# Optimization experiments

Hardware: AMD Instinct MI355X
Metric: run time of the kernel (lower is better)

## Reference

```python
import jax, jax.numpy as jnp
import numpy as np

D_MODEL = 1024
N_HEADS = 16
HEAD_DIM = D_MODEL // N_HEADS
ROPE_BASE = 10000.0


def setup_inputs() -> dict:
    key = jax.random.key(0)
    ks = jax.random.split(key, 9)
    s = 0.02
    inp = {
        "x": jax.random.normal(ks[0], (2, 2048, D_MODEL), dtype=jnp.float32),
        "Wq": jax.random.normal(ks[1], (D_MODEL, D_MODEL), dtype=jnp.float32) * s,
        "bq": jnp.zeros((D_MODEL,), dtype=jnp.float32),
        "Wk": jax.random.normal(ks[2], (D_MODEL, D_MODEL), dtype=jnp.float32) * s,
        "bk": jnp.zeros((D_MODEL,), dtype=jnp.float32),
        "Wv": jax.random.normal(ks[3], (D_MODEL, D_MODEL), dtype=jnp.float32) * s,
        "bv": jnp.zeros((D_MODEL,), dtype=jnp.float32),
        "Wo": jax.random.normal(ks[4], (D_MODEL, D_MODEL), dtype=jnp.float32) * s,
        "bo": jnp.zeros((D_MODEL,), dtype=jnp.float32),
    }
    return inp


def _rope_cos_sin(T, head_dim, dtype):
    inv_freq = 1.0 / (ROPE_BASE ** (jnp.arange(0, head_dim, 2, dtype=jnp.float32) / head_dim))
    pos = jnp.arange(T, dtype=jnp.float32)
    freqs = jnp.outer(pos, inv_freq)              # [T, head_dim/2]
    emb = jnp.concatenate([freqs, freqs], axis=-1)  # [T, head_dim]
    return jnp.cos(emb).astype(dtype), jnp.sin(emb).astype(dtype)


def _rotate_half(x):
    x1, x2 = jnp.split(x, 2, axis=-1)
    return jnp.concatenate([-x2, x1], axis=-1)


def reference(x, Wq, bq, Wk, bk, Wv, bv, Wo, bo):
    B, T, _ = x.shape
    H, Dh = N_HEADS, HEAD_DIM
    # projections (torch Linear: x @ W.T + b)
    q = (x @ Wq.T + bq).reshape(B, T, H, Dh).transpose(0, 2, 1, 3)  # [B,H,T,Dh]
    k = (x @ Wk.T + bk).reshape(B, T, H, Dh).transpose(0, 2, 1, 3)
    v = (x @ Wv.T + bv).reshape(B, T, H, Dh).transpose(0, 2, 1, 3)
    cos, sin = _rope_cos_sin(T, Dh, x.dtype)  # [T, Dh]
    cos = cos[None, None]
    sin = sin[None, None]
    q = q * cos + _rotate_half(q) * sin
    k = k * cos + _rotate_half(k) * sin
    scale = 1.0 / jnp.sqrt(jnp.asarray(Dh, dtype=x.dtype))
    attn = jnp.einsum("bhqd,bhkd->bhqk", q, k) * scale
    attn = jax.nn.softmax(attn, axis=-1)
    out = jnp.einsum("bhqk,bhkd->bhqd", attn, v)  # [B,H,T,Dh]
    out = out.transpose(0, 2, 1, 3).reshape(B, T, H * Dh)
    return out @ Wo.T + bo
```

## Files before the change

kernel.cpp:

```cpp
#include <hip/hip_runtime.h>
#include <hip/hip_bf16.h>
#include <cstdint>

#define D_MODEL 1024
#define NHEADS 16
#define HDIM 64
#define SEQ 2048
#define NBATCH 2
#define BT (NBATCH * SEQ)

typedef short bf16x8 __attribute__((ext_vector_type(8)));
typedef float f32x4 __attribute__((ext_vector_type(4)));
typedef unsigned short u16;
typedef unsigned int u32;

__device__ inline u16 f2bf(float f) {
    union { float f; u32 u; } x;
    x.f = f;
    u32 r = (x.u + 0x7fffu + ((x.u >> 16) & 1u)) >> 16;
    return (u16)r;
}

__device__ inline u32 pack2bf(float a, float b) {
    union { __hip_bfloat162 h; u32 u; } c;
    c.h = __float22bfloat162_rn(float2{a, b});
    return c.u;
}

__device__ inline float bf2f(u16 v) {
    union { u32 u; float f; } x;
    x.u = ((u32)v) << 16;
    return x.f;
}

__device__ inline void async_copy16(const u16* g, u16* l) {
    __builtin_amdgcn_global_load_lds((const __attribute__((address_space(1))) void*)g,
                                     (__attribute__((address_space(3))) void*)l, 16, 0, 0);
}

#define X4 (BT * D_MODEL / 4)
#define W4 (D_MODEL * D_MODEL / 4)
#define ROPE_N (SEQ * 32)

__global__ void prep_kernel(const float* __restrict__ x,
                            const float* __restrict__ wq, const float* __restrict__ wk,
                            const float* __restrict__ wv, const float* __restrict__ wo,
                            u16* __restrict__ xb,
                            u16* __restrict__ dq, u16* __restrict__ dk,
                            u16* __restrict__ dv, u16* __restrict__ dow,
                            float* __restrict__ cosT, float* __restrict__ sinT) {
    int idx = blockIdx.x * blockDim.x + threadIdx.x;
    if (idx < X4) {
        float4 v = ((const float4*)x)[idx];
        ushort4 o;
        o.x = f2bf(v.x); o.y = f2bf(v.y); o.z = f2bf(v.z); o.w = f2bf(v.w);
        ((ushort4*)xb)[idx] = o;
    } else if (idx < X4 + 4 * W4) {
        int j = idx - X4;
        int w = j >> 18, i = j & (W4 - 1);
        const float* s = (w == 0) ? wq : (w == 1) ? wk : (w == 2) ? wv : wo;
        u16* d = (w == 0) ? dq : (w == 1) ? dk : (w == 2) ? dv : dow;
        float4 v = ((const float4*)s)[i];
        ushort4 o;
        o.x = f2bf(v.x); o.y = f2bf(v.y); o.z = f2bf(v.z); o.w = f2bf(v.w);
        ((ushort4*)d)[i] = o;
    } else {
        int j = idx - (X4 + 4 * W4);
        if (j < ROPE_N) {
            int t = j >> 5, dd = j & 31;
            float invf = exp2f(-(float)dd * (13.287712379549449f / 32.0f));
            float ang = (float)t * invf;
            float s, c;
            sincosf(ang, &s, &c);
            cosT[t * HDIM + dd] = c;      cosT[t * HDIM + dd + 32] = c;
            sinT[t * HDIM + dd] = s;      sinT[t * HDIM + dd + 32] = s;
        }
    }
}

__device__ inline void gemm_tile_core(const u16* __restrict__ A, const u16* __restrict__ Bw,
                                      int blkM, int blkN,
                                      u16* Asmem, u16* Bsmem, f32x4 acc[4][4]) {
    const int tid = threadIdx.x;
    const int lane = tid & 63;
    const int wave = tid >> 6;
    const int waveM = wave >> 1, waveN = wave & 1;
    const int quad = lane >> 4, l16 = lane & 15;

    const int srow = tid >> 2;
    const int scol = (tid & 3) << 3;
    const u16* Ag0 = A + (size_t)(blkM * 128 + srow) * D_MODEL + scol;
    const u16* Ag1 = Ag0 + (size_t)64 * D_MODEL;
    const u16* Bg0 = Bw + (size_t)(blkN * 128 + srow) * D_MODEL + scol;
    const u16* Bg1 = Bg0 + (size_t)64 * D_MODEL;
    u16* Al0 = Asmem + srow * 32 + scol;
    u16* Al1 = Al0 + 64 * 32;
    u16* Bl0 = Bsmem + srow * 32 + scol;
    u16* Bl1 = Bl0 + 64 * 32;

    for (int k0 = 0; k0 < D_MODEL; k0 += 32) {
        __syncthreads();
        async_copy16(Ag0 + k0, Al0);
        async_copy16(Ag1 + k0, Al1);
        async_copy16(Bg0 + k0, Bl0);
        async_copy16(Bg1 + k0, Bl1);
        __syncthreads();
        bf16x8 af[4], bfr[4];
#pragma unroll
        for (int mt = 0; mt < 4; ++mt)
            af[mt] = *(const bf16x8*)&Asmem[(waveM * 64 + mt * 16 + l16) * 32 + quad * 8];
#pragma unroll
        for (int nt = 0; nt < 4; ++nt)
            bfr[nt] = *(const bf16x8*)&Bsmem[(waveN * 64 + nt * 16 + l16) * 32 + quad * 8];
#pragma unroll
        for (int mt = 0; mt < 4; ++mt)
#pragma unroll
            for (int nt = 0; nt < 4; ++nt)
                acc[mt][nt] = __builtin_amdgcn_mfma_f32_16x16x32_bf16(af[mt], bfr[nt], acc[mt][nt], 0, 0, 0);
    }
}

#define QSCALE 0.1803368801111204f
#define VPAD 132

__global__ __launch_bounds__(256) void gemm_qkv_kernel(
    const u16* __restrict__ xb,
    const u16* __restrict__ wqb, const u16* __restrict__ wkb, const u16* __restrict__ wvb,
    const float* __restrict__ bq, const float* __restrict__ bk, const float* __restrict__ bv,
    const float* __restrict__ cosT, const float* __restrict__ sinT,
    u16* __restrict__ Qb, u16* __restrict__ Kb, u16* __restrict__ VTb) {
    __shared__ __align__(16) u16 smem[128 * VPAD];
    u16* Asmem = smem;
    u16* Bsmem = smem + 128 * 32;

    const int z = blockIdx.z;
    const u16* Bw = (z == 0) ? wqb : (z == 1) ? wkb : wvb;
    const float* bias = (z == 0) ? bq : (z == 1) ? bk : bv;

    f32x4 acc[4][4];
#pragma unroll
    for (int mt = 0; mt < 4; ++mt)
#pragma unroll
        for (int nt = 0; nt < 4; ++nt)
            acc[mt][nt] = (f32x4){0.f, 0.f, 0.f, 0.f};

    gemm_tile_core(xb, Bw, blockIdx.x, blockIdx.y, Asmem, Bsmem, acc);

    const int tid = threadIdx.x;
    const int lane = tid & 63, wave = tid >> 6;
    const int waveM = wave >> 1, waveN = wave & 1;
    const int quad = lane >> 4, l16 = lane & 15;
    const int gm0 = blockIdx.x * 128 + waveM * 64 + quad * 4;
    const int gn0 = blockIdx.y * 128 + waveN * 64 + l16;

    float bvv[4];
#pragma unroll
    for (int nt = 0; nt < 4; ++nt) bvv[nt] = bias[gn0 + nt * 16];
#pragma unroll
    for (int mt = 0; mt < 4; ++mt)
#pragma unroll
        for (int nt = 0; nt < 4; ++nt)
#pragma unroll
            for (int r = 0; r < 4; ++r) acc[mt][nt][r] += bvv[nt];

    if (z < 2) {
        u16* dst = (z == 0) ? Qb : Kb;
        const float post = (z == 0) ? QSCALE : 1.0f;
#pragma unroll
        for (int mt = 0; mt < 4; ++mt) {
#pragma unroll
            for (int nt = 0; nt < 4; ++nt) {
                int n = gn0 + nt * 16;
                int d = n & 63, h = n >> 6;
#pragma unroll
                for (int r = 0; r < 4; ++r) {
                    int gm = gm0 + mt * 16 + r;
                    int t = gm & (SEQ - 1), b = gm >> 11;
                    float c = cosT[t * HDIM + d], s = sinT[t * HDIM + d];
                    float part = acc[mt][nt ^ 2][r];
                    float rot = (d < 32) ? -part : part;
                    float val = (acc[mt][nt][r] * c + rot * s) * post;
                    dst[((b * NHEADS + h) * SEQ + t) * HDIM + d] = f2bf(val);
                }
            }
        }
    } else {
        __syncthreads();
#pragma unroll
        for (int mt = 0; mt < 4; ++mt) {
            int t_local = waveM * 64 + mt * 16 + quad * 4;
#pragma unroll
            for (int nt = 0; nt < 4; ++nt) {
                int n_local = waveN * 64 + nt * 16 + l16;
                uint2 w;
                w.x = pack2bf(acc[mt][nt][0], acc[mt][nt][1]);
                w.y = pack2bf(acc[mt][nt][2], acc[mt][nt][3]);
                *(uint2*)&smem[n_local * VPAD + t_local] = w;
            }
        }
        __syncthreads();
        const int row = tid >> 1;
        const int hc = (tid & 1) * 64;
        const int n_g = blockIdx.y * 128 + row;
        const int h = n_g >> 6, d = n_g & 63;
        const int b = (blockIdx.x * 128) >> 11;
        const int t0 = ((blockIdx.x * 128) & (SEQ - 1)) + hc;
        u16* dst = &VTb[((size_t)(b * NHEADS + h) * HDIM + d) * SEQ + t0];
        const u16* src = &smem[row * VPAD + hc];
#pragma unroll
        for (int j = 0; j < 8; ++j)
            *(int4*)&dst[j * 8] = *(const int4*)&src[j * 8];
    }
}

#define LPAD 72

__global__ __launch_bounds__(256, 1) void flash_kernel(
    const u16* __restrict__ Qb, const u16* __restrict__ Kb, const u16* __restrict__ VTb,
    u16* __restrict__ Po0, u16* __restrict__ Po1, float* __restrict__ Ls) {
    __shared__ __align__(16) u16 Ks[64 * LPAD];
    __shared__ __align__(16) u16 VTs[64 * LPAD];
    __shared__ __align__(16) u16 Ps[4][64 * LPAD];

    const int tid = threadIdx.x;
    const int wave = tid >> 6, lane = tid & 63;
    const int quad = lane >> 4, l16 = lane & 15;
    const int bh = blockIdx.y;
    const int hf = blockIdx.z;
    const u16* Qh = Qb + (size_t)bh * SEQ * HDIM;
    const u16* Kh = Kb + (size_t)bh * SEQ * HDIM;
    const u16* Vh = VTb + (size_t)bh * HDIM * SEQ;
    const int qblk = blockIdx.x * 256 + wave * 64;
    u16* Pw = (u16*)Ps[wave];

    bf16x8 aq[4][2];
#pragma unroll
    for (int nt2 = 0; nt2 < 4; ++nt2)
#pragma unroll
        for (int ks = 0; ks < 2; ++ks)
            aq[nt2][ks] = *(const bf16x8*)&Qh[(qblk + nt2 * 16 + l16) * HDIM + ks * 32 + quad * 8];

    f32x4 o[4][4];
    float lsum[4] = {0.f, 0.f, 0.f, 0.f};
#pragma unroll
    for (int mt2 = 0; mt2 < 4; ++mt2)
#pragma unroll
        for (int nt = 0; nt < 4; ++nt) o[mt2][nt] = (f32x4){0.f, 0.f, 0.f, 0.f};

    const int lr = tid >> 2;
    const int lc = (tid & 3) * 16;

    const int ktEnd = (hf + 1) * (SEQ / 128);
    for (int kt = hf * (SEQ / 128); kt < ktEnd; ++kt) {
        __syncthreads();
        *(int4*)&Ks[lr * LPAD + lc] = *(const int4*)&Kh[(kt * 64 + lr) * HDIM + lc];
        *(int4*)&Ks[lr * LPAD + lc + 8] = *(const int4*)&Kh[(kt * 64 + lr) * HDIM + lc + 8];
        *(int4*)&VTs[lr * LPAD + lc] = *(const int4*)&Vh[lr * SEQ + kt * 64 + lc];
        *(int4*)&VTs[lr * LPAD + lc + 8] = *(const int4*)&Vh[lr * SEQ + kt * 64 + lc + 8];
        __syncthreads();

        f32x4 sacc[4][4];
#pragma unroll
        for (int mt = 0; mt < 4; ++mt)
#pragma unroll
            for (int nt2 = 0; nt2 < 4; ++nt2) sacc[mt][nt2] = (f32x4){0.f, 0.f, 0.f, 0.f};
#pragma unroll
        for (int ks = 0; ks < 2; ++ks) {
            bf16x8 kf[4];
#pragma unroll
            for (int mt = 0; mt < 4; ++mt)
                kf[mt] = *(const bf16x8*)&Ks[(mt * 16 + l16) * LPAD + ks * 32 + quad * 8];
#pragma unroll
            for (int mt = 0; mt < 4; ++mt)
#pragma unroll
                for (int nt2 = 0; nt2 < 4; ++nt2)
                    sacc[mt][nt2] = __builtin_amdgcn_mfma_f32_16x16x32_bf16(kf[mt], aq[nt2][ks], sacc[mt][nt2], 0, 0, 0);
        }

#pragma unroll
        for (int mt = 0; mt < 4; ++mt) {
#pragma unroll
            for (int nt2 = 0; nt2 < 4; ++nt2) {
                float p0 = __builtin_amdgcn_exp2f(sacc[mt][nt2][0]);
                float p1 = __builtin_amdgcn_exp2f(sacc[mt][nt2][1]);
                float p2 = __builtin_amdgcn_exp2f(sacc[mt][nt2][2]);
                float p3 = __builtin_amdgcn_exp2f(sacc[mt][nt2][3]);
                lsum[nt2] += (p0 + p1) + (p2 + p3);
                uint2 w;
                w.x = pack2bf(p0, p1);
                w.y = pack2bf(p2, p3);
                *(uint2*)&Pw[(nt2 * 16 + l16) * LPAD + mt * 16 + quad * 4] = w;
            }
        }

#pragma unroll
        for (int ks = 0; ks < 2; ++ks) {
            bf16x8 pf[4], vf[4];
#pragma unroll
            for (int mt2 = 0; mt2 < 4; ++mt2)
                pf[mt2] = *(const bf16x8*)&Pw[(mt2 * 16 + l16) * LPAD + ks * 32 + quad * 8];
#pragma unroll
            for (int nt = 0; nt < 4; ++nt)
                vf[nt] = *(const bf16x8*)&VTs[(nt * 16 + l16) * LPAD + ks * 32 + quad * 8];
#pragma unroll
            for (int mt2 = 0; mt2 < 4; ++mt2)
#pragma unroll
                for (int nt = 0; nt < 4; ++nt)
                    o[mt2][nt] = __builtin_amdgcn_mfma_f32_16x16x32_bf16(pf[mt2], vf[nt], o[mt2][nt], 0, 0, 0);
        }
    }

#pragma unroll
    for (int nt2 = 0; nt2 < 4; ++nt2) {
        lsum[nt2] += __shfl_xor(lsum[nt2], 16, 64);
        lsum[nt2] += __shfl_xor(lsum[nt2], 32, 64);
    }

    const int b = bh >> 4, h = bh & 15;
    u16* dst = hf ? Po1 : Po0;
#pragma unroll
    for (int mt2 = 0; mt2 < 4; ++mt2) {
#pragma unroll
        for (int nt = 0; nt < 4; ++nt) {
            int d = nt * 16 + l16;
#pragma unroll
            for (int r = 0; r < 4; ++r) {
                int q = qblk + mt2 * 16 + quad * 4 + r;
                dst[((size_t)(b * SEQ + q)) * D_MODEL + h * HDIM + d] = f2bf(o[mt2][nt][r]);
            }
        }
    }
    if (quad == 0) {
#pragma unroll
        for (int nt2 = 0; nt2 < 4; ++nt2) {
            int q = qblk + nt2 * 16 + l16;
            Ls[hf * (32 * SEQ) + bh * SEQ + q] = lsum[nt2];
        }
    }
}

__global__ __launch_bounds__(256) void gemm_out_kernel(
    const u16* __restrict__ Po0, const u16* __restrict__ Po1, const float* __restrict__ Ls,
    const u16* __restrict__ wob, const float* __restrict__ bo, float* __restrict__ dout) {
    __shared__ __align__(16) u16 Asmem[64 * 32];
    __shared__ __align__(16) u16 Bsmem[128 * 32];

    const int tid = threadIdx.x;
    const int lane = tid & 63, wave = tid >> 6;
    const int waveM = wave >> 1, waveN = wave & 1;
    const int quad = lane >> 4, l16 = lane & 15;

    f32x4 acc[2][4];
#pragma unroll
    for (int mt = 0; mt < 2; ++mt)
#pragma unroll
        for (int nt = 0; nt < 4; ++nt) acc[mt][nt] = (f32x4){0.f, 0.f, 0.f, 0.f};

    const int srow = tid >> 2;
    const int scol = (tid & 3) << 3;
    const int q = blockIdx.x * 64 + srow;
    const int b = q >> 11, t = q & (SEQ - 1);
    const size_t arow = (size_t)q * D_MODEL + scol;
    const u16* Bg0 = wob + (size_t)(blockIdx.y * 128 + srow) * D_MODEL + scol;
    const u16* Bg1 = Bg0 + (size_t)64 * D_MODEL;
    u16* Al = Asmem + srow * 32 + scol;
    u16* Bl0 = Bsmem + srow * 32 + scol;
    u16* Bl1 = Bl0 + 64 * 32;

    for (int k0 = 0; k0 < D_MODEL; k0 += 32) {
        __syncthreads();
        int h = (k0 + scol) >> 6;
        int bhq = (b * NHEADS + h) * SEQ + t;
        float l = Ls[bhq] + Ls[32 * SEQ + bhq];
        float rinv = 1.0f / l;
        uint4 A0 = *(const uint4*)&Po0[arow + k0];
        uint4 A1 = *(const uint4*)&Po1[arow + k0];
        const u16* p0 = (const u16*)&A0;
        const u16* p1 = (const u16*)&A1;
        uint4 wv;
        u32* wvp = (u32*)&wv;
#pragma unroll
        for (int j = 0; j < 4; ++j) {
            float s0 = (bf2f(p0[2 * j]) + bf2f(p1[2 * j])) * rinv;
            float s1 = (bf2f(p0[2 * j + 1]) + bf2f(p1[2 * j + 1])) * rinv;
            wvp[j] = pack2bf(s0, s1);
        }
        *(uint4*)Al = wv;
        async_copy16(Bg0 + k0, Bl0);
        async_copy16(Bg1 + k0, Bl1);
        __syncthreads();
        bf16x8 af[2], bfr[4];
#pragma unroll
        for (int mt = 0; mt < 2; ++mt)
            af[mt] = *(const bf16x8*)&Asmem[(waveM * 32 + mt * 16 + l16) * 32 + quad * 8];
#pragma unroll
        for (int nt = 0; nt < 4; ++nt)
            bfr[nt] = *(const bf16x8*)&Bsmem[(waveN * 64 + nt * 16 + l16) * 32 + quad * 8];
#pragma unroll
        for (int mt = 0; mt < 2; ++mt)
#pragma unroll
            for (int nt = 0; nt < 4; ++nt)
                acc[mt][nt] = __builtin_amdgcn_mfma_f32_16x16x32_bf16(af[mt], bfr[nt], acc[mt][nt], 0, 0, 0);
    }

    const int gm0 = blockIdx.x * 64 + waveM * 32 + quad * 4;
    const int gn0 = blockIdx.y * 128 + waveN * 64 + l16;

    float bvv[4];
#pragma unroll
    for (int nt = 0; nt < 4; ++nt) bvv[nt] = bo[gn0 + nt * 16];
#pragma unroll
    for (int mt = 0; mt < 2; ++mt)
#pragma unroll
        for (int nt = 0; nt < 4; ++nt)
#pragma unroll
            for (int r = 0; r < 4; ++r)
                dout[(size_t)(gm0 + mt * 16 + r) * D_MODEL + gn0 + nt * 16] = acc[mt][nt][r] + bvv[nt];
}

extern "C" void kernel_launch(void* const* d_in, const int* in_sizes, int n_in,
                              void* d_out, int out_size, void* d_ws, size_t ws_size,
                              hipStream_t stream) {
    const float* x  = (const float*)d_in[0];
    const float* Wq = (const float*)d_in[1];
    const float* bq = (const float*)d_in[2];
    const float* Wk = (const float*)d_in[3];
    const float* bk = (const float*)d_in[4];
    const float* Wv = (const float*)d_in[5];
    const float* bv = (const float*)d_in[6];
    const float* Wo = (const float*)d_in[7];
    const float* bo = (const float*)d_in[8];
    float* dout = (float*)d_out;

    char* ws = (char*)d_ws;
    size_t off = 0;
    u16* xb  = (u16*)(ws + off); off += (size_t)BT * D_MODEL * 2;
    u16* wqb = (u16*)(ws + off); off += (size_t)D_MODEL * D_MODEL * 2;
    u16* wkb = (u16*)(ws + off); off += (size_t)D_MODEL * D_MODEL * 2;
    u16* wvb = (u16*)(ws + off); off += (size_t)D_MODEL * D_MODEL * 2;
    u16* wob = (u16*)(ws + off); off += (size_t)D_MODEL * D_MODEL * 2;
    u16* Qb  = (u16*)(ws + off); off += (size_t)BT * D_MODEL * 2;
    u16* Kb  = (u16*)(ws + off); off += (size_t)BT * D_MODEL * 2;
    u16* VTb = (u16*)(ws + off); off += (size_t)BT * D_MODEL * 2;
    u16* Po0 = (u16*)(ws + off); off += (size_t)BT * D_MODEL * 2;
    float* cosT = (float*)(ws + off); off += (size_t)SEQ * HDIM * 4;
    float* sinT = (float*)(ws + off); off += (size_t)SEQ * HDIM * 4;
    float* Ls   = (float*)(ws + off); off += (size_t)2 * 32 * SEQ * 4;
    u16* Po1 = xb;

    const int prepN = X4 + 4 * W4 + ROPE_N;
    prep_kernel<<<dim3((prepN + 255) / 256), 256, 0, stream>>>(
        x, Wq, Wk, Wv, Wo, xb, wqb, wkb, wvb, wob, cosT, sinT);
    gemm_qkv_kernel<<<dim3(BT / 128, D_MODEL / 128, 3), 256, 0, stream>>>(
        xb, wqb, wkb, wvb, bq, bk, bv, cosT, sinT, Qb, Kb, VTb);
    flash_kernel<<<dim3(SEQ / 256, NBATCH * NHEADS, 2), 256, 0, stream>>>(
        Qb, Kb, VTb, Po0, Po1, Ls);
    gemm_out_kernel<<<dim3(BT / 64, D_MODEL / 128), 256, 0, stream>>>(
        Po0, Po1, Ls, wob, bo, dout);
}
```

Measured before the change: 218.2 us.

## Register-prefetch 128-key K/V tiles and allow two blocks per CU

The flash attention kernel now stages 128 keys per iteration instead of 64, processing them as two 64-key sub-tiles. Each pass prefetches the next K/V tile into registers before computing, which overlaps global loads with the MFMA work and halves the number of barrier pairs. Launch bounds are raised to two blocks per CU to add occupancy. In exchange, the prefetch registers raise register pressure, which could cause spills under the tighter occupancy bound, and the larger K/V tiles increase LDS use.

```diff
diff --git a/kernel.cpp b/kernel.cpp
--- a/kernel.cpp
+++ b/kernel.cpp
@@ -214,12 +214,13 @@
 }
 
 #define LPAD 72
-
-__global__ __launch_bounds__(256, 1) void flash_kernel(
+#define VSTR 136
+
+__global__ __launch_bounds__(256, 2) void flash_kernel(
     const u16* __restrict__ Qb, const u16* __restrict__ Kb, const u16* __restrict__ VTb,
     u16* __restrict__ Po0, u16* __restrict__ Po1, float* __restrict__ Ls) {
-    __shared__ __align__(16) u16 Ks[64 * LPAD];
-    __shared__ __align__(16) u16 VTs[64 * LPAD];
+    __shared__ __align__(16) u16 Ks[128 * LPAD];
+    __shared__ __align__(16) u16 VTs[64 * VSTR];
     __shared__ __align__(16) u16 Ps[4][64 * LPAD];
 
     const int tid = threadIdx.x;
@@ -247,66 +248,97 @@
 #pragma unroll
         for (int nt = 0; nt < 4; ++nt) o[mt2][nt] = (f32x4){0.f, 0.f, 0.f, 0.f};
 
-    const int lr = tid >> 2;
-    const int lc = (tid & 3) * 16;
-
-    const int ktEnd = (hf + 1) * (SEQ / 128);
-    for (int kt = hf * (SEQ / 128); kt < ktEnd; ++kt) {
-        __syncthreads();
-        *(int4*)&Ks[lr * LPAD + lc] = *(const int4*)&Kh[(kt * 64 + lr) * HDIM + lc];
-        *(int4*)&Ks[lr * LPAD + lc + 8] = *(const int4*)&Kh[(kt * 64 + lr) * HDIM + lc + 8];
-        *(int4*)&VTs[lr * LPAD + lc] = *(const int4*)&Vh[lr * SEQ + kt * 64 + lc];
-        *(int4*)&VTs[lr * LPAD + lc + 8] = *(const int4*)&Vh[lr * SEQ + kt * 64 + lc + 8];
-        __syncthreads();
-
-        f32x4 sacc[4][4];
-#pragma unroll
-        for (int mt = 0; mt < 4; ++mt)
-#pragma unroll
-            for (int nt2 = 0; nt2 < 4; ++nt2) sacc[mt][nt2] = (f32x4){0.f, 0.f, 0.f, 0.f};
-#pragma unroll
-        for (int ks = 0; ks < 2; ++ks) {
-            bf16x8 kf[4];
+    const int kr = tid >> 1, kc = (tid & 1) * 32;
+    const int vr = tid >> 2, vc = (tid & 3) * 32;
+    const u16* Kg = Kh + (size_t)kr * HDIM + kc;
+    const u16* Vg = Vh + (size_t)vr * SEQ + vc;
+    u16* Kl = Ks + kr * LPAD + kc;
+    u16* Vl = VTs + vr * VSTR + vc;
+
+    const int ktBase = hf * 8;
+    int4 kreg[4], vreg[4];
+    {
+        const u16* kg = Kg + (size_t)(ktBase * 128) * HDIM;
+        const u16* vg = Vg + ktBase * 128;
+#pragma unroll
+        for (int j = 0; j < 4; ++j) {
+            kreg[j] = *(const int4*)(kg + 8 * j);
+            vreg[j] = *(const int4*)(vg + 8 * j);
+        }
+    }
+
+    for (int i = 0; i < 8; ++i) {
+        __syncthreads();
+#pragma unroll
+        for (int j = 0; j < 4; ++j) {
+            *(int4*)(Kl + 8 * j) = kreg[j];
+            *(int4*)(Vl + 8 * j) = vreg[j];
+        }
+        __syncthreads();
+        if (i < 7) {
+            const u16* kg = Kg + (size_t)((ktBase + i + 1) * 128) * HDIM;
+            const u16* vg = Vg + (ktBase + i + 1) * 128;
+#pragma unroll
+            for (int j = 0; j < 4; ++j) {
+                kreg[j] = *(const int4*)(kg + 8 * j);
+                vreg[j] = *(const int4*)(vg + 8 * j);
+            }
+        }
+
+#pragma unroll
+        for (int sub = 0; sub < 2; ++sub) {
+            const u16* KsS = Ks + sub * 64 * LPAD;
+            const int vOff = sub * 64;
+
+            f32x4 sacc[4][4];
 #pragma unroll
             for (int mt = 0; mt < 4; ++mt)
-                kf[mt] = *(const bf16x8*)&Ks[(mt * 16 + l16) * LPAD + ks * 32 + quad * 8];
-#pragma unroll
-            for (int mt = 0; mt < 4; ++mt)
-#pragma unroll
-                for (int nt2 = 0; nt2 < 4; ++nt2)
-                    sacc[mt][nt2] = __builtin_amdgcn_mfma_f32_16x16x32_bf16(kf[mt], aq[nt2][ks], sacc[mt][nt2], 0, 0, 0);
-        }
-
-#pragma unroll
-        for (int mt = 0; mt < 4; ++mt) {
-#pragma unroll
-            for (int nt2 = 0; nt2 < 4; ++nt2) {
-                float p0 = __builtin_amdgcn_exp2f(sacc[mt][nt2][0]);
-                float p1 = __builtin_amdgcn_exp2f(sacc[mt][nt2][1]);
-                float p2 = __builtin_amdgcn_exp2f(sacc[mt][nt2][2]);
-                float p3 = __builtin_amdgcn_exp2f(sacc[mt][nt2][3]);
-                lsum[nt2] += (p0 + p1) + (p2 + p3);
-                uint2 w;
-                w.x = pack2bf(p0, p1);
-                w.y = pack2bf(p2, p3);
-                *(uint2*)&Pw[(nt2 * 16 + l16) * LPAD + mt * 16 + quad * 4] = w;
-            }
-        }
-
-#pragma unroll
-        for (int ks = 0; ks < 2; ++ks) {
-            bf16x8 pf[4], vf[4];
-#pragma unroll
-            for (int mt2 = 0; mt2 < 4; ++mt2)
-                pf[mt2] = *(const bf16x8*)&Pw[(mt2 * 16 + l16) * LPAD + ks * 32 + quad * 8];
-#pragma unroll
-            for (int nt = 0; nt < 4; ++nt)
-                vf[nt] = *(const bf16x8*)&VTs[(nt * 16 + l16) * LPAD + ks * 32 + quad * 8];
-#pragma unroll
-            for (int mt2 = 0; mt2 < 4; ++mt2)
+#pragma unroll
+                for (int nt2 = 0; nt2 < 4; ++nt2) sacc[mt][nt2] = (f32x4){0.f, 0.f, 0.f, 0.f};
+#pragma unroll
+            for (int ks = 0; ks < 2; ++ks) {
+                bf16x8 kf[4];
+#pragma unroll
+                for (int mt = 0; mt < 4; ++mt)
+                    kf[mt] = *(const bf16x8*)&KsS[(mt * 16 + l16) * LPAD + ks * 32 + quad * 8];
+#pragma unroll
+                for (int mt = 0; mt < 4; ++mt)
+#pragma unroll
+                    for (int nt2 = 0; nt2 < 4; ++nt2)
+                        sacc[mt][nt2] = __builtin_amdgcn_mfma_f32_16x16x32_bf16(kf[mt], aq[nt2][ks], sacc[mt][nt2], 0, 0, 0);
+            }
+
+#pragma unroll
+            for (int mt = 0; mt < 4; ++mt) {
+#pragma unroll
+                for (int nt2 = 0; nt2 < 4; ++nt2) {
+                    float p0 = __builtin_amdgcn_exp2f(sacc[mt][nt2][0]);
+                    float p1 = __builtin_amdgcn_exp2f(sacc[mt][nt2][1]);
+                    float p2 = __builtin_amdgcn_exp2f(sacc[mt][nt2][2]);
+                    float p3 = __builtin_amdgcn_exp2f(sacc[mt][nt2][3]);
+                    lsum[nt2] += (p0 + p1) + (p2 + p3);
+                    uint2 w;
+                    w.x = pack2bf(p0, p1);
+                    w.y = pack2bf(p2, p3);
+                    *(uint2*)&Pw[(nt2 * 16 + l16) * LPAD + mt * 16 + quad * 4] = w;
+                }
+            }
+
+#pragma unroll
+            for (int ks = 0; ks < 2; ++ks) {
+                bf16x8 pf[4], vf[4];
+#pragma unroll
+                for (int mt2 = 0; mt2 < 4; ++mt2)
+                    pf[mt2] = *(const bf16x8*)&Pw[(mt2 * 16 + l16) * LPAD + ks * 32 + quad * 8];
 #pragma unroll
                 for (int nt = 0; nt < 4; ++nt)
-                    o[mt2][nt] = __builtin_amdgcn_mfma_f32_16x16x32_bf16(pf[mt2], vf[nt], o[mt2][nt], 0, 0, 0);
+                    vf[nt] = *(const bf16x8*)&VTs[(nt * 16 + l16) * VSTR + vOff + ks * 32 + quad * 8];
+#pragma unroll
+                for (int mt2 = 0; mt2 < 4; ++mt2)
+#pragma unroll
+                    for (int nt = 0; nt < 4; ++nt)
+                        o[mt2][nt] = __builtin_amdgcn_mfma_f32_16x16x32_bf16(pf[mt2], vf[nt], o[mt2][nt], 0, 0, 0);
+            }
         }
     }
 
```

New measurement: 249.8 us. 14.5% more time.

## Split flash attention KV range four ways, swizzle P smem, pack RoPE table

Applied to the files above, without the earlier changes.

Flash attention now splits the key range into four partitions when the workspace is large enough, raising the grid from 512 to 1024 blocks. The output GEMM sums four partial outputs and their normalisers. The per-wave P buffer in shared memory switches from padded rows to an XOR-swizzled layout to avoid bank conflicts. The RoPE epilogue now reads an interleaved cos/sin float2 table and handles the rotate-half pairing explicitly per lane. The extra split adds partial-output memory traffic and extra reduction work in the output GEMM.

```diff
diff --git a/kernel.cpp b/kernel.cpp
--- a/kernel.cpp
+++ b/kernel.cpp
@@ -48,7 +48,7 @@
                             u16* __restrict__ xb,
                             u16* __restrict__ dq, u16* __restrict__ dk,
                             u16* __restrict__ dv, u16* __restrict__ dow,
-                            float* __restrict__ cosT, float* __restrict__ sinT) {
+                            float2* __restrict__ csT) {
     int idx = blockIdx.x * blockDim.x + threadIdx.x;
     if (idx < X4) {
         float4 v = ((const float4*)x)[idx];
@@ -67,13 +67,12 @@
     } else {
         int j = idx - (X4 + 4 * W4);
         if (j < ROPE_N) {
-            int t = j >> 5, dd = j & 31;
-            float invf = exp2f(-(float)dd * (13.287712379549449f / 32.0f));
+            int t = j >> 5, dm = j & 31;
+            float invf = exp2f(-(float)dm * (13.287712379549449f / 32.0f));
             float ang = (float)t * invf;
             float s, c;
             sincosf(ang, &s, &c);
-            cosT[t * HDIM + dd] = c;      cosT[t * HDIM + dd + 32] = c;
-            sinT[t * HDIM + dd] = s;      sinT[t * HDIM + dd + 32] = s;
+            csT[t * 32 + dm] = float2{c, s};
         }
     }
 }
@@ -127,7 +126,7 @@
     const u16* __restrict__ xb,
     const u16* __restrict__ wqb, const u16* __restrict__ wkb, const u16* __restrict__ wvb,
     const float* __restrict__ bq, const float* __restrict__ bk, const float* __restrict__ bv,
-    const float* __restrict__ cosT, const float* __restrict__ sinT,
+    const float2* __restrict__ csT,
     u16* __restrict__ Qb, u16* __restrict__ Kb, u16* __restrict__ VTb) {
     __shared__ __align__(16) u16 smem[128 * VPAD];
     u16* Asmem = smem;
@@ -166,22 +165,22 @@
     if (z < 2) {
         u16* dst = (z == 0) ? Qb : Kb;
         const float post = (z == 0) ? QSCALE : 1.0f;
+        const int h = 2 * blockIdx.y + waveN;
 #pragma unroll
         for (int mt = 0; mt < 4; ++mt) {
 #pragma unroll
-            for (int nt = 0; nt < 4; ++nt) {
-                int n = gn0 + nt * 16;
-                int d = n & 63, h = n >> 6;
-#pragma unroll
-                for (int r = 0; r < 4; ++r) {
-                    int gm = gm0 + mt * 16 + r;
-                    int t = gm & (SEQ - 1), b = gm >> 11;
-                    float c = cosT[t * HDIM + d], s = sinT[t * HDIM + d];
-                    float part = acc[mt][nt ^ 2][r];
-                    float rot = (d < 32) ? -part : part;
-                    float val = (acc[mt][nt][r] * c + rot * s) * post;
-                    dst[((b * NHEADS + h) * SEQ + t) * HDIM + d] = f2bf(val);
-                }
+            for (int r = 0; r < 4; ++r) {
+                int gm = gm0 + mt * 16 + r;
+                int t = gm & (SEQ - 1), b = gm >> 11;
+                float2 cs0 = csT[t * 32 + l16];
+                float2 cs1 = csT[t * 32 + 16 + l16];
+                float a0 = acc[mt][0][r], a1 = acc[mt][1][r];
+                float a2 = acc[mt][2][r], a3 = acc[mt][3][r];
+                size_t base = ((size_t)(b * NHEADS + h) * SEQ + t) * HDIM;
+                dst[base + l16]      = f2bf((a0 * cs0.x - a2 * cs0.y) * post);
+                dst[base + l16 + 16] = f2bf((a1 * cs1.x - a3 * cs1.y) * post);
+                dst[base + l16 + 32] = f2bf((a2 * cs0.x + a0 * cs0.y) * post);
+                dst[base + l16 + 48] = f2bf((a3 * cs1.x + a1 * cs1.y) * post);
             }
         }
     } else {
@@ -217,14 +216,16 @@
 
 __global__ __launch_bounds__(256, 1) void flash_kernel(
     const u16* __restrict__ Qb, const u16* __restrict__ Kb, const u16* __restrict__ VTb,
-    u16* __restrict__ Po0, u16* __restrict__ Po1, float* __restrict__ Ls) {
+    u16* __restrict__ Po0, u16* __restrict__ Po1, u16* __restrict__ Po2, u16* __restrict__ Po3,
+    float* __restrict__ Ls, int iters) {
     __shared__ __align__(16) u16 Ks[64 * LPAD];
     __shared__ __align__(16) u16 VTs[64 * LPAD];
-    __shared__ __align__(16) u16 Ps[4][64 * LPAD];
+    __shared__ __align__(16) u16 Ps[4][64 * 64];
 
     const int tid = threadIdx.x;
     const int wave = tid >> 6, lane = tid & 63;
     const int quad = lane >> 4, l16 = lane & 15;
+    const int sw = l16 & 7;
     const int bh = blockIdx.y;
     const int hf = blockIdx.z;
     const u16* Qh = Qb + (size_t)bh * SEQ * HDIM;
@@ -250,8 +251,8 @@
     const int lr = tid >> 2;
     const int lc = (tid & 3) * 16;
 
-    const int ktEnd = (hf + 1) * (SEQ / 128);
-    for (int kt = hf * (SEQ / 128); kt < ktEnd; ++kt) {
+    const int kt0 = hf * iters;
+    for (int kt = kt0; kt < kt0 + iters; ++kt) {
         __syncthreads();
         *(int4*)&Ks[lr * LPAD + lc] = *(const int4*)&Kh[(kt * 64 + lr) * HDIM + lc];
         *(int4*)&Ks[lr * LPAD + lc + 8] = *(const int4*)&Kh[(kt * 64 + lr) * HDIM + lc + 8];
@@ -289,7 +290,8 @@
                 uint2 w;
                 w.x = pack2bf(p0, p1);
                 w.y = pack2bf(p2, p3);
-                *(uint2*)&Pw[(nt2 * 16 + l16) * LPAD + mt * 16 + quad * 4] = w;
+                int chunk = (mt * 2 + (quad >> 1)) ^ sw;
+                *(uint2*)&Pw[(nt2 * 16 + l16) * 64 + chunk * 8 + (quad & 1) * 4] = w;
             }
         }
 
@@ -297,8 +299,10 @@
         for (int ks = 0; ks < 2; ++ks) {
             bf16x8 pf[4], vf[4];
 #pragma unroll
-            for (int mt2 = 0; mt2 < 4; ++mt2)
-                pf[mt2] = *(const bf16x8*)&Pw[(mt2 * 16 + l16) * LPAD + ks * 32 + quad * 8];
+            for (int mt2 = 0; mt2 < 4; ++mt2) {
+                int chunk = (ks * 4 + quad) ^ sw;
+                pf[mt2] = *(const bf16x8*)&Pw[(mt2 * 16 + l16) * 64 + chunk * 8];
+            }
 #pragma unroll
             for (int nt = 0; nt < 4; ++nt)
                 vf[nt] = *(const bf16x8*)&VTs[(nt * 16 + l16) * LPAD + ks * 32 + quad * 8];
@@ -317,7 +321,7 @@
     }
 
     const int b = bh >> 4, h = bh & 15;
-    u16* dst = hf ? Po1 : Po0;
+    u16* dst = (hf == 0) ? Po0 : (hf == 1) ? Po1 : (hf == 2) ? Po2 : Po3;
 #pragma unroll
     for (int mt2 = 0; mt2 < 4; ++mt2) {
 #pragma unroll
@@ -340,7 +344,9 @@
 }
 
 __global__ __launch_bounds__(256) void gemm_out_kernel(
-    const u16* __restrict__ Po0, const u16* __restrict__ Po1, const float* __restrict__ Ls,
+    const u16* __restrict__ Po0, const u16* __restrict__ Po1,
+    const u16* __restrict__ Po2, const u16* __restrict__ Po3,
+    const float* __restrict__ Ls, int nsplit,
     const u16* __restrict__ wob, const float* __restrict__ bo, float* __restrict__ dout) {
     __shared__ __align__(16) u16 Asmem[64 * 32];
     __shared__ __align__(16) u16 Bsmem[128 * 32];
@@ -372,19 +378,28 @@
         int h = (k0 + scol) >> 6;
         int bhq = (b * NHEADS + h) * SEQ + t;
         float l = Ls[bhq] + Ls[32 * SEQ + bhq];
+        if (nsplit == 4) l += Ls[2 * 32 * SEQ + bhq] + Ls[3 * 32 * SEQ + bhq];
         float rinv = 1.0f / l;
         uint4 A0 = *(const uint4*)&Po0[arow + k0];
         uint4 A1 = *(const uint4*)&Po1[arow + k0];
         const u16* p0 = (const u16*)&A0;
         const u16* p1 = (const u16*)&A1;
+        float sv[8];
+#pragma unroll
+        for (int e = 0; e < 8; ++e) sv[e] = bf2f(p0[e]) + bf2f(p1[e]);
+        if (nsplit == 4) {
+            uint4 A2 = *(const uint4*)&Po2[arow + k0];
+            uint4 A3 = *(const uint4*)&Po3[arow + k0];
+            const u16* p2 = (const u16*)&A2;
+            const u16* p3 = (const u16*)&A3;
+#pragma unroll
+            for (int e = 0; e < 8; ++e) sv[e] += bf2f(p2[e]) + bf2f(p3[e]);
+        }
         uint4 wv;
         u32* wvp = (u32*)&wv;
 #pragma unroll
-        for (int j = 0; j < 4; ++j) {
-            float s0 = (bf2f(p0[2 * j]) + bf2f(p1[2 * j])) * rinv;
-            float s1 = (bf2f(p0[2 * j + 1]) + bf2f(p1[2 * j + 1])) * rinv;
-            wvp[j] = pack2bf(s0, s1);
-        }
+        for (int j = 0; j < 4; ++j)
+            wvp[j] = pack2bf(sv[2 * j] * rinv, sv[2 * j + 1] * rinv);
         *(uint4*)Al = wv;
         async_copy16(Bg0 + k0, Bl0);
         async_copy16(Bg1 + k0, Bl1);
@@ -443,18 +458,21 @@
     u16* Kb  = (u16*)(ws + off); off += (size_t)BT * D_MODEL * 2;
     u16* VTb = (u16*)(ws + off); off += (size_t)BT * D_MODEL * 2;
     u16* Po0 = (u16*)(ws + off); off += (size_t)BT * D_MODEL * 2;
-    float* cosT = (float*)(ws + off); off += (size_t)SEQ * HDIM * 4;
-    float* sinT = (float*)(ws + off); off += (size_t)SEQ * HDIM * 4;
-    float* Ls   = (float*)(ws + off); off += (size_t)2 * 32 * SEQ * 4;
+    float2* csT = (float2*)(ws + off); off += (size_t)SEQ * 32 * 8;
+    float* Ls   = (float*)(ws + off); off += (size_t)4 * 32 * SEQ * 4;
     u16* Po1 = xb;
+    u16* Po2 = (u16*)(ws + off); size_t off4 = off + (size_t)BT * D_MODEL * 2;
+    u16* Po3 = (u16*)(ws + off4); off4 += (size_t)BT * D_MODEL * 2;
+    const int nsplit = (ws_size >= off4) ? 4 : 2;
+    if (nsplit == 2) { Po2 = Po0; Po3 = Po1; }
 
     const int prepN = X4 + 4 * W4 + ROPE_N;
     prep_kernel<<<dim3((prepN + 255) / 256), 256, 0, stream>>>(
-        x, Wq, Wk, Wv, Wo, xb, wqb, wkb, wvb, wob, cosT, sinT);
+        x, Wq, Wk, Wv, Wo, xb, wqb, wkb, wvb, wob, csT);
     gemm_qkv_kernel<<<dim3(BT / 128, D_MODEL / 128, 3), 256, 0, stream>>>(
-        xb, wqb, wkb, wvb, bq, bk, bv, cosT, sinT, Qb, Kb, VTb);
-    flash_kernel<<<dim3(SEQ / 256, NBATCH * NHEADS, 2), 256, 0, stream>>>(
-        Qb, Kb, VTb, Po0, Po1, Ls);
+        xb, wqb, wkb, wvb, bq, bk, bv, csT, Qb, Kb, VTb);
+    flash_kernel<<<dim3(SEQ / 256, NBATCH * NHEADS, nsplit), 256, 0, stream>>>(
+        Qb, Kb, VTb, Po0, Po1, Po2, Po3, Ls, 32 / nsplit);
     gemm_out_kernel<<<dim3(BT / 64, D_MODEL / 128), 256, 0, stream>>>(
-        Po0, Po1, Ls, wob, bo, dout);
-}
+        Po0, Po1, Po2, Po3, Ls, nsplit, wob, bo, dout);
+}
```

Result: slower. 227.4 us (+4.2%).
